# Optimization experiments

Measured on AMD Instinct MI355X. Metric: run time of the kernel, lower is better.

Reference implementation:

```python
import jax, jax.numpy as jnp
import numpy as np

S, B, C, H, E = 4096, 2, 256, 8, 131072
CC = C // H


def setup_inputs() -> dict:
    key = jax.random.key(0)
    ks = jax.random.split(key, 12)
    sc = 0.02
    inp = {
        "x": jax.random.normal(ks[0], (S, B, C), jnp.float32),
        "q_id": jax.random.randint(ks[1], (E,), 0, S, jnp.int32),
        "k_id": jax.random.randint(ks[2], (E,), 0, S, jnp.int32),
        "Wq": jax.random.normal(ks[3], (C, C), jnp.float32) * sc,
        "bq": jnp.zeros((C,), jnp.float32),
        "Wk": jax.random.normal(ks[4], (C, C), jnp.float32) * sc,
        "bk": jnp.zeros((C,), jnp.float32),
        "Wv": jax.random.normal(ks[5], (C, C), jnp.float32) * sc,
        "bv": jnp.zeros((C,), jnp.float32),
        "Wx": jax.random.normal(ks[6], (C, C), jnp.float32) * sc,
        "bx": jnp.zeros((C,), jnp.float32),
    }
    return inp


def reference(x, q_id, k_id, Wq, bq, Wk, bk, Wv, bv, Wx, bx):
    s, b, c = x.shape
    cc = c // H
    # qkv projections (torch Linear: x @ W.T + b)
    q = (x @ Wq.T + bq).reshape(s, b, H, cc)
    k = (x @ Wk.T + bk).reshape(s, b, H, cc)
    v = (x @ Wv.T + bv).reshape(s, b, H, cc)
    # per-edge scores: gather along sequence axis by edge ids
    qk = jnp.einsum('ebhc,ebhc->ebh', q[q_id], k[k_id])[..., None]  # [E,b,h,1]
    qk = qk / jnp.sqrt(jnp.asarray(cc, x.dtype))
    eqk = jnp.exp(qk - jnp.max(qk))  # global max, as in original
    # scatter-add softmax normalizer and weighted sum over edges
    d = jnp.zeros((s, b, H, 1), x.dtype).at[q_id].add(eqk)
    out = jnp.zeros((s, b, H, cc), x.dtype).at[q_id].add(eqk * v[k_id])
    out = (out / d).reshape(s, b, c)
    return out @ Wx.T + bx
```

## Files before the change

### kernel.cpp

```cpp
#include <hip/hip_runtime.h>

constexpr int S_  = 4096;
constexpr int B_  = 2;
constexpr int C_  = 256;
constexpr int H_  = 8;
constexpr int E_  = 131072;
constexpr int CC_ = 32;
constexpr int MR  = S_ * B_;

typedef __attribute__((ext_vector_type(8))) short bf16x8_t;
typedef __attribute__((ext_vector_type(4))) float f32x4_t;

__device__ __forceinline__ unsigned short f2bf(float f) {
    unsigned int u = __float_as_uint(f);
    u += 0x7fffu + ((u >> 16) & 1u);
    return (unsigned short)(u >> 16);
}
__device__ __forceinline__ float bflo(unsigned int u) { return __uint_as_float(u << 16); }
__device__ __forceinline__ float bfhi(unsigned int u) { return __uint_as_float(u & 0xffff0000u); }

__device__ __forceinline__ void cast8(const float* __restrict__ src, unsigned short* __restrict__ dst, int i) {
    const float4* s = (const float4*)src + (size_t)i * 2;
    float4 a = s[0], b = s[1];
    uint4 o;
    o.x = (unsigned)f2bf(a.x) | ((unsigned)f2bf(a.y) << 16);
    o.y = (unsigned)f2bf(a.z) | ((unsigned)f2bf(a.w) << 16);
    o.z = (unsigned)f2bf(b.x) | ((unsigned)f2bf(b.y) << 16);
    o.w = (unsigned)f2bf(b.z) | ((unsigned)f2bf(b.w) << 16);
    *((uint4*)dst + i) = o;
}


__global__ __launch_bounds__(256) void prep_kernel(
        const int* __restrict__ q_id, int* __restrict__ count,
        const float* __restrict__ x, unsigned short* __restrict__ xb,
        const float* __restrict__ Wq, const float* __restrict__ Wk,
        const float* __restrict__ Wv, const float* __restrict__ Wx,
        unsigned short* __restrict__ Wb) {
    const int bid = blockIdx.x, tid = threadIdx.x;
    if (bid < 512) {
        atomicAdd(&count[q_id[bid * 256 + tid]], 1);
    } else if (bid < 1536) {
        cast8(x, xb, (bid - 512) * 256 + tid);
    } else {
        int idx = bid - 1536;
        int z = idx >> 5;
        const float* src = (z == 0) ? Wq : (z == 1) ? Wk : (z == 2) ? Wv : Wx;
        cast8(src, Wb + (size_t)z * (C_ * C_), (idx & 31) * 256 + tid);
    }
}


__global__ __launch_bounds__(1024) void scan_kernel(const int* __restrict__ count,
                                                    int* __restrict__ base,
                                                    int* __restrict__ cursor) {
    __shared__ int wsums[16];
    const int t = threadIdx.x, lane = t & 63, w = t >> 6;
    int c0 = count[4 * t + 0], c1 = count[4 * t + 1];
    int c2 = count[4 * t + 2], c3 = count[4 * t + 3];
    int tsum = c0 + c1 + c2 + c3;
    int x = tsum;
#pragma unroll
    for (int off = 1; off < 64; off <<= 1) {
        int y = __shfl_up(x, off);
        if (lane >= off) x += y;
    }
    if (lane == 63) wsums[w] = x;
    __syncthreads();
    if (t == 0) {
        int run = 0;
#pragma unroll
        for (int i = 0; i < 16; ++i) { int v = wsums[i]; wsums[i] = run; run += v; }
        base[S_] = run;
    }
    __syncthreads();
    int excl = x - tsum + wsums[w];
    int b0 = excl, b1 = b0 + c0, b2 = b1 + c1, b3 = b2 + c2;
    base[4 * t + 0] = b0; base[4 * t + 1] = b1;
    base[4 * t + 2] = b2; base[4 * t + 3] = b3;
    cursor[4 * t + 0] = b0; cursor[4 * t + 1] = b1;
    cursor[4 * t + 2] = b2; cursor[4 * t + 3] = b3;
}


template <int NB, bool BF16OUT>
__device__ __forceinline__ void gemm_body(
        const unsigned short* __restrict__ A, const unsigned short* __restrict__ W,
        const float* __restrict__ bias,
        unsigned short* __restrict__ outb, float* __restrict__ outf,
        int ostride, int ooff, int bm, int bn) {
    constexpr int NT = NB / 32;
    __shared__ __align__(16) unsigned short As[128][72];
    __shared__ __align__(16) unsigned short Bs[NB][72];
    const int tid = threadIdx.x;
    const int lane = tid & 63, wave = tid >> 6;
    const int wm = wave >> 1, wn = wave & 1;
    const int l16 = lane & 15, quad = lane >> 4;
    f32x4_t acc[4][NT] = {};

    for (int k0 = 0; k0 < C_; k0 += 64) {
#pragma unroll
        for (int i = 0; i < 4; ++i) {
            int l = i * 256 + tid;
            int r = l >> 3, c8 = (l & 7) << 3;
            *(uint4*)&As[r][c8] = *(const uint4*)&A[(size_t)(bm + r) * C_ + k0 + c8];
        }
#pragma unroll
        for (int i = 0; i < NT; ++i) {
            int l = i * 256 + tid;
            int r = l >> 3, c8 = (l & 7) << 3;
            *(uint4*)&Bs[r][c8] = *(const uint4*)&W[(size_t)(bn + r) * C_ + k0 + c8];
        }
        __syncthreads();
#pragma unroll
        for (int ks = 0; ks < 2; ++ks) {
            bf16x8_t af[4], bf[NT];
#pragma unroll
            for (int t = 0; t < 4; ++t)
                af[t] = *(const bf16x8_t*)&As[wm * 64 + t * 16 + l16][ks * 32 + quad * 8];
#pragma unroll
            for (int t = 0; t < NT; ++t)
                bf[t] = *(const bf16x8_t*)&Bs[wn * (NB / 2) + t * 16 + l16][ks * 32 + quad * 8];
#pragma unroll
            for (int i = 0; i < 4; ++i)
#pragma unroll
                for (int j = 0; j < NT; ++j)
                    acc[i][j] = __builtin_amdgcn_mfma_f32_16x16x32_bf16(af[i], bf[j], acc[i][j], 0, 0, 0);
        }
        __syncthreads();
    }

    float bcol[NT];
#pragma unroll
    for (int tn = 0; tn < NT; ++tn)
        bcol[tn] = bias[bn + wn * (NB / 2) + tn * 16 + l16];

    char* buf = (char*)&As[0][0];
#pragma unroll
    for (int tm = 0; tm < 4; ++tm) {
        __syncthreads();
        const int lrow = wm * 16 + quad * 4;
#pragma unroll
        for (int tn = 0; tn < NT; ++tn) {
            const int col = wn * (NB / 2) + tn * 16 + l16;
#pragma unroll
            for (int r = 0; r < 4; ++r) {
                float val = acc[tm][tn][r] + bcol[tn];
                if (BF16OUT) ((unsigned short*)(buf + (size_t)(lrow + r) * 272))[col] = f2bf(val);
                else         ((float*)(buf + (size_t)(lrow + r) * 272))[col] = val;
            }
        }
        __syncthreads();
#pragma unroll
        for (int i = 0; i < 2; ++i) {
            int f = tid * 2 + i;
            int lr = f >> 4, cc = f & 15;
            int grow = bm + (lr >> 4) * 64 + tm * 16 + (lr & 15);
            if (BF16OUT)
                *(uint4*)&outb[(size_t)grow * ostride + ooff + bn + cc * 8] =
                    *(const uint4*)(buf + (size_t)lr * 272 + cc * 16);
            else
                *(float4*)&outf[(size_t)grow * C_ + bn + cc * 4] =
                    *(const float4*)(buf + (size_t)lr * 272 + cc * 16);
        }
    }
}


__global__ __launch_bounds__(256) void scatter_qkv_kernel(
        const int* __restrict__ q_id, const int* __restrict__ k_id,
        int* __restrict__ cursor, int* __restrict__ koff_sorted,
        const unsigned short* __restrict__ xb, const unsigned short* __restrict__ Wb,
        const float* __restrict__ bq, const float* __restrict__ bk, const float* __restrict__ bv,
        unsigned short* __restrict__ qb, unsigned short* __restrict__ kvb) {
    const int bid = blockIdx.x;
    if (bid < 512) {
        int e = bid * 256 + threadIdx.x;
        int pos = atomicAdd(&cursor[q_id[e]], 1);
        koff_sorted[pos] = k_id[e] << 10;
        return;
    }
    int gb = bid - 512;
    int z = gb >> 7, rem = gb & 127;
    int bm = (rem >> 1) * 128, bn = (rem & 1) * 128;
    const unsigned short* W = Wb + (size_t)z * (C_ * C_);
    const float* bias = (z == 0) ? bq : (z == 1) ? bk : bv;
    unsigned short* outb = (z == 0) ? qb : kvb;
    int stride = (z == 0) ? 256 : 512;
    int off = (z == 2) ? 256 : 0;
    gemm_body<128, true>(xb, W, bias, outb, nullptr, stride, off, bm, bn);
}


__global__ __launch_bounds__(256) void attn_edge(
        const unsigned short* __restrict__ qb, const unsigned short* __restrict__ kvb,
        const int* __restrict__ base, const int* __restrict__ koff,
        unsigned short* __restrict__ attnb) {
    __shared__ float red[2][64][9];
    const int lane = threadIdx.x & 63;
    const int wave = threadIdx.x >> 6;
    const int rw = wave >> 1, part = wave & 1;
    const int s = blockIdx.x * 2 + rw;
    const int half = lane >> 5, hl = lane & 31;
    const int e0 = __builtin_amdgcn_readfirstlane(base[s]);
    const int e1 = __builtin_amdgcn_readfirstlane(base[s + 1]);

    const uint4 qq = *((const uint4*)(qb + (size_t)(s * 2 + half) * C_) + hl);
    const float q0 = bflo(qq.x), q1 = bfhi(qq.x), q2 = bflo(qq.y), q3 = bfhi(qq.y);
    const float q4 = bflo(qq.z), q5 = bfhi(qq.z), q6 = bflo(qq.w), q7 = bfhi(qq.w);

    float a0 = 0.f, a1 = 0.f, a2 = 0.f, a3 = 0.f, a4 = 0.f, a5 = 0.f, a6 = 0.f, a7 = 0.f;
    float wsum = 0.f;
    const float scale = 0.17677669529663687f;

    for (int j = e0 + part; j < e1; j += 2) {
        const int kb = koff[j];
        const uint4* kvp = (const uint4*)(kvb + kb + half * 512);
        const uint4 kk = kvp[hl];
        const uint4 vv = kvp[32 + hl];
        float p = q0 * bflo(kk.x) + q1 * bfhi(kk.x)
                + q2 * bflo(kk.y) + q3 * bfhi(kk.y)
                + q4 * bflo(kk.z) + q5 * bfhi(kk.z)
                + q6 * bflo(kk.w) + q7 * bfhi(kk.w);
        p += __shfl_xor(p, 1);
        p += __shfl_xor(p, 2);
        const float w = __expf(p * scale);
        a0 = fmaf(w, bflo(vv.x), a0); a1 = fmaf(w, bfhi(vv.x), a1);
        a2 = fmaf(w, bflo(vv.y), a2); a3 = fmaf(w, bfhi(vv.y), a3);
        a4 = fmaf(w, bflo(vv.z), a4); a5 = fmaf(w, bfhi(vv.z), a5);
        a6 = fmaf(w, bflo(vv.w), a6); a7 = fmaf(w, bfhi(vv.w), a7);
        wsum += w;
    }

    if (part == 1) {
        float* r = red[rw][lane];
        r[0] = a0; r[1] = a1; r[2] = a2; r[3] = a3;
        r[4] = a4; r[5] = a5; r[6] = a6; r[7] = a7; r[8] = wsum;
    }
    __syncthreads();
    if (part == 0) {
        const float* r = red[rw][lane];
        a0 += r[0]; a1 += r[1]; a2 += r[2]; a3 += r[3];
        a4 += r[4]; a5 += r[5]; a6 += r[6]; a7 += r[7]; wsum += r[8];
        const float inv = 1.0f / wsum;
        uint4 o;
        o.x = (unsigned)f2bf(a0 * inv) | ((unsigned)f2bf(a1 * inv) << 16);
        o.y = (unsigned)f2bf(a2 * inv) | ((unsigned)f2bf(a3 * inv) << 16);
        o.z = (unsigned)f2bf(a4 * inv) | ((unsigned)f2bf(a5 * inv) << 16);
        o.w = (unsigned)f2bf(a6 * inv) | ((unsigned)f2bf(a7 * inv) << 16);
        *((uint4*)(attnb + (size_t)(s * 2 + half) * C_) + hl) = o;
    }
}


__global__ __launch_bounds__(256) void gemm_proj(
        const unsigned short* __restrict__ attnb, const unsigned short* __restrict__ Wxb,
        const float* __restrict__ bx, float* __restrict__ out) {
    gemm_body<64, false>(attnb, Wxb, bx, nullptr, out, 0, 0, blockIdx.x * 128, blockIdx.y * 64);
}


extern "C" void kernel_launch(void* const* d_in, const int* in_sizes, int n_in,
                              void* d_out, int out_size, void* d_ws, size_t ws_size,
                              hipStream_t stream) {
    const float* x  = (const float*)d_in[0];
    const int* q_id = (const int*)d_in[1];
    const int* k_id = (const int*)d_in[2];
    const float* Wq = (const float*)d_in[3];
    const float* bq = (const float*)d_in[4];
    const float* Wk = (const float*)d_in[5];
    const float* bk = (const float*)d_in[6];
    const float* Wv = (const float*)d_in[7];
    const float* bv = (const float*)d_in[8];
    const float* Wx = (const float*)d_in[9];
    const float* bx = (const float*)d_in[10];
    float* out = (float*)d_out;

    char* ws = (char*)d_ws;
    unsigned short* xb    = (unsigned short*)ws;                 ws += (size_t)MR * C_ * 2;
    unsigned short* qb    = (unsigned short*)ws;                 ws += (size_t)MR * C_ * 2;
    unsigned short* kvb   = (unsigned short*)ws;                 ws += (size_t)MR * 512 * 2;
    unsigned short* attnb = (unsigned short*)ws;                 ws += (size_t)MR * C_ * 2;
    unsigned short* Wb    = (unsigned short*)ws;                 ws += (size_t)4 * C_ * C_ * 2;
    int* count       = (int*)ws;                                 ws += S_ * 4;
    int* base        = (int*)ws;                                 ws += (S_ + 1) * 4;
    int* cursor      = (int*)ws;                                 ws += S_ * 4;
    int* koff_sorted = (int*)ws;

    hipMemsetAsync(count, 0, S_ * sizeof(int), stream);
    prep_kernel<<<1664, 256, 0, stream>>>(q_id, count, x, xb, Wq, Wk, Wv, Wx, Wb);
    scan_kernel<<<1, 1024, 0, stream>>>(count, base, cursor);
    scatter_qkv_kernel<<<896, 256, 0, stream>>>(q_id, k_id, cursor, koff_sorted,
                                                xb, Wb, bq, bk, bv, qb, kvb);
    attn_edge<<<S_ / 2, 256, 0, stream>>>(qb, kvb, base, koff_sorted, attnb);
    gemm_proj<<<dim3(MR / 128, C_ / 64), 256, 0, stream>>>(
        attnb, Wb + (size_t)3 * C_ * C_, bx, out);
}
```

Baseline: 157.2 us.

## Software-pipeline edge gathers with batched index loads and double-buffered K/V prefetch

The per-row attention loop now loads up to 64 edge offsets at once into lanes, one per lane, and broadcasts each with readlane. This removes the dependent scalar index load that came before every K/V gather. K/V fetches are double-buffered so the next two edges' loads are in flight while the current edge's dot product and exp run, which hides gather latency. The GEMM epilogue also changes its bf16 store mapping when NB differs from 128, so narrower tiles issue one store per thread. The cost is more registers for the two buffered K/V pairs and more complex tail handling.

```diff
diff --git a/kernel.cpp b/kernel.cpp
--- a/kernel.cpp
+++ b/kernel.cpp
@@ -106,7 +106,7 @@
             *(uint4*)&As[r][c8] = *(const uint4*)&A[(size_t)(bm + r) * C_ + k0 + c8];
         }
 #pragma unroll
-        for (int i = 0; i < NT; ++i) {
+        for (int i = 0; i < NB / 32; ++i) {
             int l = i * 256 + tid;
             int r = l >> 3, c8 = (l & 7) << 3;
             *(uint4*)&Bs[r][c8] = *(const uint4*)&W[(size_t)(bn + r) * C_ + k0 + c8];
@@ -156,12 +156,23 @@
             int f = tid * 2 + i;
             int lr = f >> 4, cc = f & 15;
             int grow = bm + (lr >> 4) * 64 + tm * 16 + (lr & 15);
-            if (BF16OUT)
-                *(uint4*)&outb[(size_t)grow * ostride + ooff + bn + cc * 8] =
-                    *(const uint4*)(buf + (size_t)lr * 272 + cc * 16);
-            else
+            if (BF16OUT) {
+                if (NB == 128 || i == 0) {
+                    int f2 = (NB == 128) ? f : tid;
+                    lr = f2 >> 3; cc = f2 & 7;
+                    grow = bm + (lr >> 4) * 64 + tm * 16 + (lr & 15);
+                    if (NB == 128) { lr = f2 >> 4; cc = f2 & 15; grow = bm + (lr >> 4) * 64 + tm * 16 + (lr & 15);
+                        *(uint4*)&outb[(size_t)grow * ostride + ooff + bn + cc * 8] =
+                            *(const uint4*)(buf + (size_t)lr * 272 + cc * 16);
+                    } else {
+                        *(uint4*)&outb[(size_t)grow * ostride + ooff + bn + cc * 8] =
+                            *(const uint4*)(buf + (size_t)lr * 272 + cc * 16);
+                    }
+                }
+            } else {
                 *(float4*)&outf[(size_t)grow * C_ + bn + cc * 4] =
                     *(const float4*)(buf + (size_t)lr * 272 + cc * 16);
+            }
         }
     }
 }
@@ -213,11 +224,7 @@
     float wsum = 0.f;
     const float scale = 0.17677669529663687f;
 
-    for (int j = e0 + part; j < e1; j += 2) {
-        const int kb = koff[j];
-        const uint4* kvp = (const uint4*)(kvb + kb + half * 512);
-        const uint4 kk = kvp[hl];
-        const uint4 vv = kvp[32 + hl];
+    auto edge = [&](const uint4& kk, const uint4& vv) {
         float p = q0 * bflo(kk.x) + q1 * bfhi(kk.x)
                 + q2 * bflo(kk.y) + q3 * bfhi(kk.y)
                 + q4 * bflo(kk.z) + q5 * bfhi(kk.z)
@@ -230,6 +237,30 @@
         a4 = fmaf(w, bflo(vv.z), a4); a5 = fmaf(w, bfhi(vv.z), a5);
         a6 = fmaf(w, bflo(vv.w), a6); a7 = fmaf(w, bfhi(vv.w), a7);
         wsum += w;
+    };
+    auto fetch = [&](int my, int t, uint4& kk, uint4& vv) {
+        int o = __builtin_amdgcn_readlane(my, part + 2 * t);
+        const uint4* p = (const uint4*)(kvb + o + half * 512);
+        kk = p[hl]; vv = p[32 + hl];
+    };
+
+    for (int b0 = e0; b0 < e1; b0 += 64) {
+        const int m = min(64, e1 - b0);
+        const int my = koff[b0 + ((lane < m) ? lane : 0)];
+        const int nm = (m > part) ? ((m - part + 1) >> 1) : 0;
+        uint4 kka = {}, vva = {}, kkb = {}, vvb = {};
+        if (nm > 0) fetch(my, 0, kka, vva);
+        if (nm > 1) fetch(my, 1, kkb, vvb);
+        int t = 0;
+        for (; t + 3 < nm; t += 2) {
+            edge(kka, vva);
+            fetch(my, t + 2, kka, vva);
+            edge(kkb, vvb);
+            fetch(my, t + 3, kkb, vvb);
+        }
+        if (t < nm)     edge(kka, vva);
+        if (t + 1 < nm) edge(kkb, vvb);
+        if (t + 2 < nm) { fetch(my, t + 2, kka, vva); edge(kka, vva); }
     }
 
     if (part == 1) {
```

Result: no change. 155.5 us (-1.1%).
